# Optimization experiments

Measured on AMD Instinct MI355X. Metric: run time of the kernel, lower is better.

Reference implementation:

```python
import jax, jax.numpy as jnp
import numpy as np
import math

B, T, C, NH = 4, 2048, 1024, 16
D = C // NH  # 64, rotary_dim == D

def _rope_tables():
    inv_freq = 1.0 / (10000.0 ** (np.arange(0, D, 2, dtype=np.float32) / D))
    t = np.arange(T, dtype=np.float32)
    freqs = np.outer(t, inv_freq)                 # [T, D/2]
    emb = np.concatenate([freqs, freqs], axis=-1)  # [T, D]
    return jnp.asarray(np.cos(emb))[None], jnp.asarray(np.sin(emb))[None]  # [1,T,D]

def setup_inputs() -> dict:
    key = jax.random.key(0)
    ks = jax.random.split(key, 3)
    x = jax.random.normal(ks[0], (B, T, C), dtype=jnp.float32)
    w_attn = jax.random.normal(ks[1], (3 * C, C), dtype=jnp.float32) * (1.0 / math.sqrt(C))
    b_attn = jnp.zeros((3 * C,), dtype=jnp.float32)
    w_proj = jax.random.normal(ks[2], (C, C), dtype=jnp.float32) * (1.0 / math.sqrt(C))
    b_proj = jnp.zeros((C,), dtype=jnp.float32)
    cos, sin = _rope_tables()
    return {"x": x, "w_attn": w_attn, "b_attn": b_attn,
            "w_proj": w_proj, "b_proj": b_proj, "cos": cos, "sin": sin}

def _rotate_half(u):
    u1, u2 = jnp.split(u, 2, axis=-1)
    return jnp.concatenate([-u2, u1], axis=-1)

def reference(x, w_attn, b_attn, w_proj, b_proj, cos, sin):
    Bx, Tx, Cx = x.shape
    nh, d = NH, Cx // NH
    # fused QKV projection (torch Linear: y = x @ W^T + b)
    qkv = x @ w_attn.T + b_attn                      # [B,T,3C]
    q, k, v = jnp.split(qkv, 3, axis=-1)
    q = q.reshape(Bx, Tx, nh, d).transpose(0, 2, 1, 3)  # [B,nh,T,d]
    k = k.reshape(Bx, Tx, nh, d).transpose(0, 2, 1, 3)
    v = v.reshape(Bx, Tx, nh, d).transpose(0, 2, 1, 3)
    # RoPE (rotary_dim == d, full head)
    c = cos[:, None, :, :]  # [1,1,T,d]
    s = sin[:, None, :, :]
    q = q * c + _rotate_half(q) * s
    k = k * c + _rotate_half(k) * s
    # naive causal attention
    scores = jnp.einsum("bhqd,bhkd->bhqk", q, k) / math.sqrt(d)
    causal = jnp.tril(jnp.ones((Tx, Tx), dtype=bool))
    scores = jnp.where(causal[None, None], scores, -jnp.inf)
    att = jax.nn.softmax(scores, axis=-1)
    y = jnp.einsum("bhqk,bhkd->bhqd", att, v)        # [B,nh,T,d]
    y = y.transpose(0, 2, 1, 3).reshape(Bx, Tx, Cx)
    return y @ w_proj.T + b_proj
```

## Files before the change

### kernel.cpp

```cpp
#include <hip/hip_runtime.h>

typedef __bf16 bf16_t;
typedef bf16_t bf16x8 __attribute__((ext_vector_type(8)));
typedef bf16_t bf16x4 __attribute__((ext_vector_type(4)));
typedef float f32x4 __attribute__((ext_vector_type(4)));

constexpr int BATCH = 4, SEQ = 2048, CH = 1024, NHEAD = 16, HD = 64;
constexpr int BM = 128, BN = 128, BKK = 32;

#define LGKM_FENCE() __asm__ __volatile__("s_waitcnt lgkmcnt(0)" ::: "memory")
#define VM_FENCE() __asm__ __volatile__("s_waitcnt vmcnt(0)" ::: "memory")
#define REORDER_FENCE() __asm__ __volatile__("" ::: "memory")

__device__ __forceinline__ void g2lds16(const bf16_t* g, bf16_t* l) {
  __builtin_amdgcn_global_load_lds((__attribute__((address_space(1))) void*)(g),
                                   (__attribute__((address_space(3))) void*)(l),
                                   16, 0, 0);
}

__device__ __forceinline__ f32x4 mfma16(bf16x8 a, bf16x8 b, f32x4 c) {
  return __builtin_amdgcn_mfma_f32_16x16x32_bf16(a, b, c, 0, 0, 0);
}

__global__ __launch_bounds__(256) void cvt_kernel(const float4* __restrict__ src,
                                                  ushort4* __restrict__ dst, int n4) {
  int i = blockIdx.x * 256 + threadIdx.x;
  if (i >= n4) return;
  float4 f = src[i];
  ushort4 o;
  o.x = __builtin_bit_cast(unsigned short, (bf16_t)f.x);
  o.y = __builtin_bit_cast(unsigned short, (bf16_t)f.y);
  o.z = __builtin_bit_cast(unsigned short, (bf16_t)f.z);
  o.w = __builtin_bit_cast(unsigned short, (bf16_t)f.w);
  dst[i] = o;
}

__device__ __forceinline__ void gemm_mainloop(const bf16_t* __restrict__ A,
                                              const bf16_t* __restrict__ W, int Kdim,
                                              int m0, int n0,
                                              bf16_t* As, bf16_t* Bs,
                                              f32x4 acc[4][4]) {
  const int tid = threadIdx.x;
  const int lane = tid & 63, w = tid >> 6;
  const int quad = lane >> 4, l16 = lane & 15;
  const int wm = (w >> 1) << 6, wn = (w & 1) << 6;
  const int srow = (w << 5) + (lane >> 2);
  const int scol = (lane & 3) << 3;
  const bf16_t* ga0 = A + (size_t)(m0 + srow) * Kdim + scol;
  const bf16_t* ga1 = A + (size_t)(m0 + srow + 16) * Kdim + scol;
  const bf16_t* gb0 = W + (size_t)(n0 + srow) * Kdim + scol;
  const bf16_t* gb1 = W + (size_t)(n0 + srow + 16) * Kdim + scol;
  bf16_t* la0 = As + srow * BKK + scol;
  bf16_t* la1 = As + (srow + 16) * BKK + scol;
  bf16_t* lb0 = Bs + srow * BKK + scol;
  bf16_t* lb1 = Bs + (srow + 16) * BKK + scol;
  for (int k0 = 0; k0 < Kdim; k0 += BKK) {
    g2lds16(ga0 + k0, la0);
    g2lds16(ga1 + k0, la1);
    g2lds16(gb0 + k0, lb0);
    g2lds16(gb1 + k0, lb1);
    VM_FENCE();
    __syncthreads();
    bf16x8 av[4], bv[4];
#pragma unroll
    for (int i = 0; i < 4; i++)
      av[i] = *(const bf16x8*)&As[(wm + i * 16 + l16) * BKK + quad * 8];
#pragma unroll
    for (int i = 0; i < 4; i++)
      bv[i] = *(const bf16x8*)&Bs[(wn + i * 16 + l16) * BKK + quad * 8];
#pragma unroll
    for (int mi = 0; mi < 4; mi++)
#pragma unroll
      for (int ni = 0; ni < 4; ni++)
        acc[mi][ni] = mfma16(av[mi], bv[ni], acc[mi][ni]);
    __syncthreads();
  }
}

constexpr float SCL = 0.125f * 1.44269504089f;

__global__ __launch_bounds__(256) void qkv_rope_kernel(
    const bf16_t* __restrict__ X, const bf16_t* __restrict__ Wa,
    const float* __restrict__ ba, const float* __restrict__ cosT,
    const float* __restrict__ sinT, bf16_t* __restrict__ Q,
    bf16_t* __restrict__ Ko, bf16_t* __restrict__ VT) {
  constexpr int TSTRIDE = 68;
  __shared__ __align__(16) char smem[4 * 64 * TSTRIDE * 2];
  bf16_t* As = (bf16_t*)smem;
  bf16_t* Bs = As + BM * BKK;

  f32x4 acc[4][4];
#pragma unroll
  for (int i = 0; i < 4; i++)
#pragma unroll
    for (int j = 0; j < 4; j++) acc[i][j] = (f32x4){0.f, 0.f, 0.f, 0.f};

  const int n0 = blockIdx.x * BN, m0 = blockIdx.y * BM;
  gemm_mainloop(X, Wa, CH, m0, n0, As, Bs, acc);

  const int tid = threadIdx.x, lane = tid & 63, w = tid >> 6;
  const int quad = lane >> 4, l16 = lane & 15;
  const int wm = (w >> 1) << 6, wn = (w & 1) << 6;
  const int nbase = n0 + wn;
  const int part = nbase >> 10;
  const int h = (nbase & 1023) >> 6;
  const int mbase = m0 + wm;
  const int bb = mbase >> 11;
  const size_t headbase = ((size_t)(bb * NHEAD + h)) * SEQ * HD;

  if (part < 2) {
    bf16_t* O = (part == 0) ? Q : Ko;
    const float post = (part == 0) ? SCL : 1.0f;
#pragma unroll
    for (int mi = 0; mi < 4; mi++)
#pragma unroll
      for (int r = 0; r < 4; r++) {
        int m = mbase + mi * 16 + quad * 4 + r;
        int t = m & (SEQ - 1);
        const float* cr = cosT + t * HD;
        const float* sr = sinT + t * HD;
        size_t rowo = headbase + (size_t)t * HD;
#pragma unroll
        for (int ni = 0; ni < 2; ni++) {
          int d0 = ni * 16 + l16, d1 = d0 + 32;
          float v0 = acc[mi][ni][r] + ba[nbase + d0];
          float v1 = acc[mi][ni + 2][r] + ba[nbase + d1];
          float r0 = (v0 * cr[d0] - v1 * sr[d0]) * post;
          float r1 = (v1 * cr[d1] + v0 * sr[d1]) * post;
          O[rowo + d0] = (bf16_t)r0;
          O[rowo + d1] = (bf16_t)r1;
        }
      }
  } else {
    bf16_t* tb = (bf16_t*)smem + w * 64 * TSTRIDE;
    int t0 = mbase & (SEQ - 1);
#pragma unroll
    for (int mi = 0; mi < 4; mi++)
#pragma unroll
      for (int ni = 0; ni < 4; ni++) {
        int d = ni * 16 + l16;
        float bias = ba[nbase + d];
#pragma unroll
        for (int r = 0; r < 4; r++) {
          float v = acc[mi][ni][r] + bias;
          tb[d * TSTRIDE + mi * 16 + quad * 4 + r] = (bf16_t)v;
        }
      }
    LGKM_FENCE();
    int half = lane >> 5, l5 = lane & 31;
    size_t vbase = ((size_t)(bb * NHEAD + h)) * HD * SEQ;
#pragma unroll
    for (int it = 0; it < 32; it++) {
      int d = it * 2 + half;
      unsigned int val = *(const unsigned int*)&tb[d * TSTRIDE + l5 * 2];
      *(unsigned int*)&VT[vbase + (size_t)d * SEQ + t0 + l5 * 2] = val;
    }
  }
}

__device__ __forceinline__ void sm_update(f32x4 (&s)[4], float& lr,
                                          bf16_t* Prow, int quad,
                                          int swz, bool domask, int lim) {
  if (domask) {
#pragma unroll
    for (int ni = 0; ni < 4; ni++)
#pragma unroll
      for (int r = 0; r < 4; r++)
        if (ni * 16 + r > lim) s[ni][r] = -1e30f;
  }
  float sum = 0.f;
#pragma unroll
  for (int ni = 0; ni < 4; ni++) {
    float p0 = __builtin_exp2f(s[ni][0]);
    float p1 = __builtin_exp2f(s[ni][1]);
    float p2 = __builtin_exp2f(s[ni][2]);
    float p3 = __builtin_exp2f(s[ni][3]);
    bf16x4 pk = {(bf16_t)p0, (bf16_t)p1, (bf16_t)p2, (bf16_t)p3};
    *(bf16x4*)&Prow[(((ni << 2) | quad) ^ (swz << 1)) << 2] = pk;
    sum += (p0 + p1) + (p2 + p3);
  }
  lr += sum;
}

__global__ __launch_bounds__(256) void flash_kernel(const bf16_t* __restrict__ Q,
                                                    const bf16_t* __restrict__ Kg,
                                                    const bf16_t* __restrict__ VT,
                                                    bf16_t* __restrict__ att) {
  __shared__ __align__(16) bf16_t Ks[2][64 * 64];
  __shared__ __align__(16) bf16_t Vs[2][64 * 64];
  __shared__ __align__(16) bf16_t Pt[4][16 * 64];
  const int tid = threadIdx.x, w = tid >> 6, lane = tid & 63;
  const int quad = lane >> 4, l16 = lane & 15;
  const int qb = 15 - ((int)blockIdx.x >> 6);
  const int bh = (int)blockIdx.x & 63;
  const bf16_t* Qp = Q + (size_t)bh * SEQ * HD;
  const bf16_t* Kb = Kg + (size_t)bh * SEQ * HD;
  const bf16_t* Vb = VT + (size_t)bh * HD * SEQ;
  const int grow = lane >> 3;
  const int gj8 = ((lane & 7) ^ grow) * 8;
  const int i0 = w * 2;
  const int sw = l16 & 7;
  const int swz = l16 >> 1;
  const int bloc = bh >> 4, hh = bh & 15;
  bf16_t* Pw = &Pt[w][l16 * 64];
  const int rs0 = (quad ^ swz) << 3;
  const int rs1 = ((4 + quad) ^ swz) << 3;

  auto stage = [&](int kcs, int b) {
#pragma unroll
    for (int ii = 0; ii < 2; ii++) {
      int i = i0 + ii;
      g2lds16(Kb + (size_t)(kcs + i * 8 + grow) * HD + gj8, &Ks[b][(i * 64 + lane) * 8]);
      g2lds16(Vb + (size_t)(i * 8 + grow) * SEQ + kcs + gj8, &Vs[b][(i * 64 + lane) * 8]);
    }
  };

  const int q0 = qb * 128;
  const int mA = q0 + w * 16, mB = mA + 64;
  bf16x8 aqA0 = *(const bf16x8*)&Qp[(size_t)(mA + l16) * HD + quad * 8];
  bf16x8 aqA1 = *(const bf16x8*)&Qp[(size_t)(mA + l16) * HD + 32 + quad * 8];
  bf16x8 aqB0 = *(const bf16x8*)&Qp[(size_t)(mB + l16) * HD + quad * 8];
  bf16x8 aqB1 = *(const bf16x8*)&Qp[(size_t)(mB + l16) * HD + 32 + quad * 8];
  float lrA = 0.f, lrB = 0.f;
  f32x4 yA[4], yB[4];
#pragma unroll
  for (int ni = 0; ni < 4; ni++) {
    yA[ni] = (f32x4){0.f, 0.f, 0.f, 0.f};
    yB[ni] = (f32x4){0.f, 0.f, 0.f, 0.f};
  }
  const int nch = 2 * qb + 2;

  stage(0, 0);
  VM_FENCE();
  __syncthreads();

  for (int c = 0; c < nch; ++c) {
    const int kc = c * 64, buf = c & 1;
    if (c + 1 < nch) stage(kc + 64, buf ^ 1);
    const bool doA = (c + 1 < nch);
    f32x4 sA[4], sB[4];
#pragma unroll
    for (int ni = 0; ni < 4; ni++) {
      bf16x8 k0 = *(const bf16x8*)&Ks[buf][((ni * 16 + l16) * 8 + (quad ^ sw)) * 8];
      bf16x8 k1 = *(const bf16x8*)&Ks[buf][((ni * 16 + l16) * 8 + ((4 + quad) ^ sw)) * 8];
      f32x4 z = (f32x4){0.f, 0.f, 0.f, 0.f};
      sB[ni] = mfma16(k1, aqB1, mfma16(k0, aqB0, z));
      if (doA) sA[ni] = mfma16(k1, aqA1, mfma16(k0, aqA0, z));
    }
    sm_update(sB, lrB, Pw, quad, swz, c == nch - 1, mB + l16 - kc - quad * 4);
    LGKM_FENCE();
    {
      bf16x8 pB0 = *(const bf16x8*)&Pw[rs0];
      bf16x8 pB1 = *(const bf16x8*)&Pw[rs1];
#pragma unroll
      for (int ni = 0; ni < 4; ni++) {
        bf16x8 v0 = *(const bf16x8*)&Vs[buf][((ni * 16 + l16) * 8 + (quad ^ sw)) * 8];
        bf16x8 v1 = *(const bf16x8*)&Vs[buf][((ni * 16 + l16) * 8 + ((4 + quad) ^ sw)) * 8];
        yB[ni] = mfma16(v1, pB1, mfma16(v0, pB0, yB[ni]));
      }
    }
    if (doA) {
      REORDER_FENCE();
      sm_update(sA, lrA, Pw, quad, swz, c == nch - 2, mA + l16 - kc - quad * 4);
      LGKM_FENCE();
      bf16x8 pA0 = *(const bf16x8*)&Pw[rs0];
      bf16x8 pA1 = *(const bf16x8*)&Pw[rs1];
#pragma unroll
      for (int ni = 0; ni < 4; ni++) {
        bf16x8 v0 = *(const bf16x8*)&Vs[buf][((ni * 16 + l16) * 8 + (quad ^ sw)) * 8];
        bf16x8 v1 = *(const bf16x8*)&Vs[buf][((ni * 16 + l16) * 8 + ((4 + quad) ^ sw)) * 8];
        yA[ni] = mfma16(v1, pA1, mfma16(v0, pA0, yA[ni]));
      }
    }
    VM_FENCE();
    __syncthreads();
  }

  lrA += __shfl_xor(lrA, 16);
  lrA += __shfl_xor(lrA, 32);
  lrB += __shfl_xor(lrB, 16);
  lrB += __shfl_xor(lrB, 32);
  float invA = 1.f / lrA, invB = 1.f / lrB;
  size_t rbA = ((size_t)bloc * SEQ + mA + l16) * CH + hh * HD + quad * 4;
  size_t rbB = ((size_t)bloc * SEQ + mB + l16) * CH + hh * HD + quad * 4;
#pragma unroll
  for (int ni = 0; ni < 4; ni++) {
    bf16x4 oA = {(bf16_t)(yA[ni][0] * invA), (bf16_t)(yA[ni][1] * invA),
                 (bf16_t)(yA[ni][2] * invA), (bf16_t)(yA[ni][3] * invA)};
    bf16x4 oB = {(bf16_t)(yB[ni][0] * invB), (bf16_t)(yB[ni][1] * invB),
                 (bf16_t)(yB[ni][2] * invB), (bf16_t)(yB[ni][3] * invB)};
    *(bf16x4*)&att[rbA + ni * 16] = oA;
    *(bf16x4*)&att[rbB + ni * 16] = oB;
  }
}

__global__ __launch_bounds__(256) void proj_kernel(const bf16_t* __restrict__ A,
                                                   const bf16_t* __restrict__ Wp,
                                                   const float* __restrict__ bp,
                                                   float* __restrict__ out) {
  __shared__ __align__(16) bf16_t As[BM * BKK];
  __shared__ __align__(16) bf16_t Bs[BN * BKK];
  f32x4 acc[4][4];
#pragma unroll
  for (int i = 0; i < 4; i++)
#pragma unroll
    for (int j = 0; j < 4; j++) acc[i][j] = (f32x4){0.f, 0.f, 0.f, 0.f};
  const int n0 = blockIdx.x * BN, m0 = blockIdx.y * BM;
  gemm_mainloop(A, Wp, CH, m0, n0, As, Bs, acc);
  const int tid = threadIdx.x, lane = tid & 63, w = tid >> 6;
  const int quad = lane >> 4, l16 = lane & 15;
  const int wm = (w >> 1) << 6, wn = (w & 1) << 6;
  const int nbase = n0 + wn, mbase = m0 + wm;
#pragma unroll
  for (int mi = 0; mi < 4; mi++)
#pragma unroll
    for (int r = 0; r < 4; r++) {
      int m = mbase + mi * 16 + quad * 4 + r;
#pragma unroll
      for (int ni = 0; ni < 4; ni++) {
        int n = nbase + ni * 16 + l16;
        out[(size_t)m * CH + n] = acc[mi][ni][r] + bp[n];
      }
    }
}

extern "C" void kernel_launch(void* const* d_in, const int* in_sizes, int n_in,
                              void* d_out, int out_size, void* d_ws, size_t ws_size,
                              hipStream_t stream) {
  const float* x      = (const float*)d_in[0];
  const float* w_attn = (const float*)d_in[1];
  const float* b_attn = (const float*)d_in[2];
  const float* w_proj = (const float*)d_in[3];
  const float* b_proj = (const float*)d_in[4];
  const float* cosT   = (const float*)d_in[5];
  const float* sinT   = (const float*)d_in[6];
  float* out = (float*)d_out;

  bf16_t* xbf  = (bf16_t*)d_ws;
  bf16_t* wabf = xbf + (size_t)8192 * 1024;
  bf16_t* wpbf = wabf + (size_t)3072 * 1024;
  bf16_t* Qb   = wpbf + (size_t)1024 * 1024;
  bf16_t* Kb   = Qb + (size_t)8388608;
  bf16_t* VTb  = Kb + (size_t)8388608;
  bf16_t* attb = VTb + (size_t)8388608;

  cvt_kernel<<<8192, 256, 0, stream>>>((const float4*)x, (ushort4*)xbf, 2097152);
  cvt_kernel<<<3072, 256, 0, stream>>>((const float4*)w_attn, (ushort4*)wabf, 786432);
  cvt_kernel<<<1024, 256, 0, stream>>>((const float4*)w_proj, (ushort4*)wpbf, 262144);
  qkv_rope_kernel<<<dim3(24, 64), 256, 0, stream>>>(xbf, wabf, b_attn, cosT, sinT,
                                                    Qb, Kb, VTb);
  flash_kernel<<<dim3(1024), 256, 0, stream>>>(Qb, Kb, VTb, attb);
  proj_kernel<<<dim3(8, 64), 256, 0, stream>>>(attb, wpbf, b_proj, out);
}
```

Before: 293.3 us.

## Pair light and heavy 64-row query tiles per flash block for causal balance

The flash kernel no longer processes one 128-row query block with two interleaved 64-row halves sharing each K/V chunk. Each block now processes two 64-row tiles one after the other: tile 31-p and then tile p. Every block therefore does the same number of causal K/V chunks, which is meant to remove load imbalance across the grid. In exchange, K/V tiles are staged separately for each query tile, so global and LDS traffic and barrier count per unit of work go up, and the overlap between the two tiles' softmax and MFMA work is lost.

```diff
diff --git a/kernel.cpp b/kernel.cpp
--- a/kernel.cpp
+++ b/kernel.cpp
@@ -191,7 +191,7 @@
   __shared__ __align__(16) bf16_t Pt[4][16 * 64];
   const int tid = threadIdx.x, w = tid >> 6, lane = tid & 63;
   const int quad = lane >> 4, l16 = lane & 15;
-  const int qb = 15 - ((int)blockIdx.x >> 6);
+  const int p = (int)blockIdx.x >> 6;
   const int bh = (int)blockIdx.x & 63;
   const bf16_t* Qp = Q + (size_t)bh * SEQ * HD;
   const bf16_t* Kb = Kg + (size_t)bh * SEQ * HD;
@@ -215,82 +215,56 @@
     }
   };
 
-  const int q0 = qb * 128;
-  const int mA = q0 + w * 16, mB = mA + 64;
-  bf16x8 aqA0 = *(const bf16x8*)&Qp[(size_t)(mA + l16) * HD + quad * 8];
-  bf16x8 aqA1 = *(const bf16x8*)&Qp[(size_t)(mA + l16) * HD + 32 + quad * 8];
-  bf16x8 aqB0 = *(const bf16x8*)&Qp[(size_t)(mB + l16) * HD + quad * 8];
-  bf16x8 aqB1 = *(const bf16x8*)&Qp[(size_t)(mB + l16) * HD + 32 + quad * 8];
-  float lrA = 0.f, lrB = 0.f;
-  f32x4 yA[4], yB[4];
-#pragma unroll
-  for (int ni = 0; ni < 4; ni++) {
-    yA[ni] = (f32x4){0.f, 0.f, 0.f, 0.f};
-    yB[ni] = (f32x4){0.f, 0.f, 0.f, 0.f};
-  }
-  const int nch = 2 * qb + 2;
-
-  stage(0, 0);
-  VM_FENCE();
-  __syncthreads();
-
-  for (int c = 0; c < nch; ++c) {
-    const int kc = c * 64, buf = c & 1;
-    if (c + 1 < nch) stage(kc + 64, buf ^ 1);
-    const bool doA = (c + 1 < nch);
-    f32x4 sA[4], sB[4];
-#pragma unroll
-    for (int ni = 0; ni < 4; ni++) {
-      bf16x8 k0 = *(const bf16x8*)&Ks[buf][((ni * 16 + l16) * 8 + (quad ^ sw)) * 8];
-      bf16x8 k1 = *(const bf16x8*)&Ks[buf][((ni * 16 + l16) * 8 + ((4 + quad) ^ sw)) * 8];
-      f32x4 z = (f32x4){0.f, 0.f, 0.f, 0.f};
-      sB[ni] = mfma16(k1, aqB1, mfma16(k0, aqB0, z));
-      if (doA) sA[ni] = mfma16(k1, aqA1, mfma16(k0, aqA0, z));
-    }
-    sm_update(sB, lrB, Pw, quad, swz, c == nch - 1, mB + l16 - kc - quad * 4);
-    LGKM_FENCE();
-    {
-      bf16x8 pB0 = *(const bf16x8*)&Pw[rs0];
-      bf16x8 pB1 = *(const bf16x8*)&Pw[rs1];
+  for (int sp = 0; sp < 2; ++sp) {
+    const int j = sp ? p : 31 - p;
+    const int m = j * 64 + w * 16;
+    const int nch = j + 1;
+    bf16x8 aq0 = *(const bf16x8*)&Qp[(size_t)(m + l16) * HD + quad * 8];
+    bf16x8 aq1 = *(const bf16x8*)&Qp[(size_t)(m + l16) * HD + 32 + quad * 8];
+    float lr = 0.f;
+    f32x4 y[4];
+#pragma unroll
+    for (int ni = 0; ni < 4; ni++) y[ni] = (f32x4){0.f, 0.f, 0.f, 0.f};
+
+    stage(0, 0);
+    VM_FENCE();
+    __syncthreads();
+
+    for (int c = 0; c < nch; ++c) {
+      const int kc = c * 64, buf = c & 1;
+      if (c + 1 < nch) stage(kc + 64, buf ^ 1);
+      f32x4 s[4];
+#pragma unroll
+      for (int ni = 0; ni < 4; ni++) {
+        bf16x8 k0 = *(const bf16x8*)&Ks[buf][((ni * 16 + l16) * 8 + (quad ^ sw)) * 8];
+        bf16x8 k1 = *(const bf16x8*)&Ks[buf][((ni * 16 + l16) * 8 + ((4 + quad) ^ sw)) * 8];
+        f32x4 z = (f32x4){0.f, 0.f, 0.f, 0.f};
+        s[ni] = mfma16(k1, aq1, mfma16(k0, aq0, z));
+      }
+      sm_update(s, lr, Pw, quad, swz, c == nch - 1, m + l16 - kc - quad * 4);
+      LGKM_FENCE();
+      bf16x8 p0 = *(const bf16x8*)&Pw[rs0];
+      bf16x8 p1 = *(const bf16x8*)&Pw[rs1];
 #pragma unroll
       for (int ni = 0; ni < 4; ni++) {
         bf16x8 v0 = *(const bf16x8*)&Vs[buf][((ni * 16 + l16) * 8 + (quad ^ sw)) * 8];
         bf16x8 v1 = *(const bf16x8*)&Vs[buf][((ni * 16 + l16) * 8 + ((4 + quad) ^ sw)) * 8];
-        yB[ni] = mfma16(v1, pB1, mfma16(v0, pB0, yB[ni]));
-      }
-    }
-    if (doA) {
-      REORDER_FENCE();
-      sm_update(sA, lrA, Pw, quad, swz, c == nch - 2, mA + l16 - kc - quad * 4);
-      LGKM_FENCE();
-      bf16x8 pA0 = *(const bf16x8*)&Pw[rs0];
-      bf16x8 pA1 = *(const bf16x8*)&Pw[rs1];
-#pragma unroll
-      for (int ni = 0; ni < 4; ni++) {
-        bf16x8 v0 = *(const bf16x8*)&Vs[buf][((ni * 16 + l16) * 8 + (quad ^ sw)) * 8];
-        bf16x8 v1 = *(const bf16x8*)&Vs[buf][((ni * 16 + l16) * 8 + ((4 + quad) ^ sw)) * 8];
-        yA[ni] = mfma16(v1, pA1, mfma16(v0, pA0, yA[ni]));
-      }
-    }
-    VM_FENCE();
-    __syncthreads();
-  }
-
-  lrA += __shfl_xor(lrA, 16);
-  lrA += __shfl_xor(lrA, 32);
-  lrB += __shfl_xor(lrB, 16);
-  lrB += __shfl_xor(lrB, 32);
-  float invA = 1.f / lrA, invB = 1.f / lrB;
-  size_t rbA = ((size_t)bloc * SEQ + mA + l16) * CH + hh * HD + quad * 4;
-  size_t rbB = ((size_t)bloc * SEQ + mB + l16) * CH + hh * HD + quad * 4;
-#pragma unroll
-  for (int ni = 0; ni < 4; ni++) {
-    bf16x4 oA = {(bf16_t)(yA[ni][0] * invA), (bf16_t)(yA[ni][1] * invA),
-                 (bf16_t)(yA[ni][2] * invA), (bf16_t)(yA[ni][3] * invA)};
-    bf16x4 oB = {(bf16_t)(yB[ni][0] * invB), (bf16_t)(yB[ni][1] * invB),
-                 (bf16_t)(yB[ni][2] * invB), (bf16_t)(yB[ni][3] * invB)};
-    *(bf16x4*)&att[rbA + ni * 16] = oA;
-    *(bf16x4*)&att[rbB + ni * 16] = oB;
+        y[ni] = mfma16(v1, p1, mfma16(v0, p0, y[ni]));
+      }
+      VM_FENCE();
+      __syncthreads();
+    }
+
+    lr += __shfl_xor(lr, 16);
+    lr += __shfl_xor(lr, 32);
+    float inv = 1.f / lr;
+    size_t rb = ((size_t)bloc * SEQ + m + l16) * CH + hh * HD + quad * 4;
+#pragma unroll
+    for (int ni = 0; ni < 4; ni++) {
+      bf16x4 o = {(bf16_t)(y[ni][0] * inv), (bf16_t)(y[ni][1] * inv),
+                  (bf16_t)(y[ni][2] * inv), (bf16_t)(y[ni][3] * inv)};
+      *(bf16x4*)&att[rb + ni * 16] = o;
+    }
   }
 }
 
```

New measurement: 280.9 us. 4.2% less time.
